# Kernel tuning notes

Hardware: AMD Instinct MI355X
Metric: run time of the kernel (lower is better)

The kernel has to match this reference:

```python
import jax, jax.numpy as jnp
import numpy as np
from math import sqrt

B, S, I, H, O, R = 32, 2048, 128, 512, 64, 1
ALPHA = 0.1


def setup_inputs() -> dict:
    key = jax.random.key(0)
    ks = jax.random.split(key, 7)
    x = jax.random.normal(ks[0], (B, S, I), dtype=jnp.float32)
    input_projective = jax.random.normal(ks[1], (H, R), dtype=jnp.float32) / sqrt(H)
    input_receptive = jax.random.normal(ks[2], (I, R), dtype=jnp.float32) / sqrt(I)
    rec_projective = jax.random.normal(ks[3], (H, R), dtype=jnp.float32) / sqrt(H)
    rec_receptive = jax.random.normal(ks[4], (H, R), dtype=jnp.float32) / sqrt(H)
    bound = 1.0 / sqrt(H)
    readout_w = jax.random.uniform(ks[5], (O, H), minval=-bound, maxval=bound, dtype=jnp.float32)
    readout_b = jax.random.uniform(ks[6], (O,), minval=-bound, maxval=bound, dtype=jnp.float32)
    return {
        "x": x,
        "input_projective": input_projective,
        "input_receptive": input_receptive,
        "rec_projective": rec_projective,
        "rec_receptive": rec_receptive,
        "readout_w": readout_w,
        "readout_b": readout_b,
    }


def reference(x, input_projective, input_receptive, rec_projective, rec_receptive, readout_w, readout_b):
    # Precompute input drive for all steps using the low-rank factorization:
    # x_in[b,s,h] = x[b,s,:] @ input_receptive @ input_projective.T
    x_in = jnp.einsum("bsi,ir,hr->bsh", x, input_receptive, input_projective)

    def step(h, xin_t):
        # r_in = (J @ h.T).T with J = P @ R.T  ->  h @ R @ P.T (low-rank)
        r_in = (h @ rec_receptive) @ rec_projective.T
        dh = -h + jax.nn.relu(r_in + xin_t)  # activation = nlfun (relu)
        h = h + ALPHA * dh                   # Euler hidden update
        out_t = h @ readout_w.T + readout_b
        return h, out_t

    h0 = jnp.zeros((x.shape[0], rec_projective.shape[0]), dtype=x.dtype)
    _, out = jax.lax.scan(step, h0, jnp.swapaxes(x_in, 0, 1))  # scan over time
    return jnp.swapaxes(out, 0, 1)  # [B, S, O]
```

## Files before the change

kernel.cpp:

```cpp
#include <hip/hip_runtime.h>


#define B_ 32
#define S_ 2048
#define I_ 128
#define H_ 512
#define O_ 64

typedef __attribute__((ext_vector_type(8))) short bf16x8;
typedef __attribute__((ext_vector_type(4))) float f32x4;

__device__ __forceinline__ unsigned short f2bf(float f) {
  unsigned int b = __float_as_uint(f);
  b += 0x7FFFu + ((b >> 16) & 1u);
  return (unsigned short)(b >> 16);
}
__device__ __forceinline__ float bf2f(unsigned short s) {
  return __uint_as_float(((unsigned)s) << 16);
}
__device__ __forceinline__ unsigned pack_bf(float lo, float hi) {
  unsigned a = (__float_as_uint(lo) + 0x8000u) >> 16;
  unsigned b = (__float_as_uint(hi) + 0x8000u) & 0xFFFF0000u;
  return a | b;
}

#define DPP_ADD(s, CTRL) \
  s += __int_as_float(__builtin_amdgcn_update_dpp(0, __float_as_int(s), CTRL, 0xF, 0xF, true))

#define RL(s, L) __int_as_float(__builtin_amdgcn_readlane(__float_as_int(s), (L)))

__device__ __forceinline__ void gload16(const void* g, void* l) {
  __builtin_amdgcn_global_load_lds(
      (const __attribute__((address_space(1))) unsigned int*)g,
      (__attribute__((address_space(3))) unsigned int*)l, 16, 0, 0);
}
#define WAITVM(N) asm volatile("s_waitcnt vmcnt(" #N ")" ::: "memory")
#define SCHEDB() __builtin_amdgcn_sched_barrier(0)

#define OFF_SU 0
#define OFF_SV 1920
#define OFF_RP 3456
#define OFF_IP 5504
#define OFF_SW 7552
#define OFF_XS 48512
#define SMEM_BYTES 146816

__device__ __forceinline__ int swz(int row, int col) {
  return row * 64 + (col ^ ((((unsigned)row >> 2) & 3) << 4));
}

__global__ __launch_bounds__(512, 1) void k_fused(
    const float* __restrict__ x, const float* __restrict__ ipj,
    const float* __restrict__ irc, const float* __restrict__ rpj,
    const float* __restrict__ rrc, const float* __restrict__ Wr,
    const float* __restrict__ bias, float* __restrict__ out) {
  extern __shared__ __align__(16) char smem[];
  float* su = (float*)(smem + OFF_SU);
  float* sV = (float*)(smem + OFF_SV);
  float* srp = (float*)(smem + OFF_RP);
  float* sip = (float*)(smem + OFF_IP);
  unsigned short* sw = (unsigned short*)(smem + OFF_SW);
  unsigned short* sBF = (unsigned short*)(smem + OFF_XS);
  float* xsf = (float*)(smem + OFF_XS);

  const int tid = threadIdx.x;
  const int wv = tid >> 6;
  const int lane = tid & 63;
  const int b = blockIdx.x >> 3;
  const int g = blockIdx.x & 7;
  const int r0 = g * 256;

  f32x4 cv0 = *(const f32x4*)(irc + 4 * (lane & 7));
  f32x4 cv1 = *(const f32x4*)(irc + 4 * (lane & 7) + 32);
  f32x4 cv2 = *(const f32x4*)(irc + 4 * (lane & 7) + 64);
  f32x4 cv3 = *(const f32x4*)(irc + 4 * (lane & 7) + 96);
  float rpv[8], ipv[8], rrv[8];
  #pragma unroll
  for (int k = 0; k < 8; k++) {
    int h = lane + 64 * k;
    rpv[k] = rpj[h]; ipv[k] = ipj[h]; rrv[k] = 0.1f * rrc[h];
  }
  if (tid < 96) su[384 + tid] = 0.f;
  if (tid < 80) sV[304 + tid] = 0.f;

#define ISSUE(c) do { \
    int tc_ = r0 - 128 + (c) * 64 + wv * 8; if (tc_ < 0) tc_ = 0; \
    const float* gs_ = x + ((size_t)b * S_ + tc_) * I_ + lane * 4; \
    char* ld_ = (char*)xsf + ((c) % 3) * 32768 + wv * 4096; \
    gload16(gs_,       ld_); \
    gload16(gs_ + 256, ld_ + 1024); \
    gload16(gs_ + 512, ld_ + 2048); \
    gload16(gs_ + 768, ld_ + 3072); \
  } while (0)

#define COMPUTE(c) do { \
    const float* bp_ = xsf + ((c) % 3) * 8192 + (wv * 8 + (lane >> 3)) * 128 + (lane & 7) * 4; \
    f32x4 x0_ = *(const f32x4*)(bp_); \
    f32x4 x1_ = *(const f32x4*)(bp_ + 32); \
    f32x4 x2_ = *(const f32x4*)(bp_ + 64); \
    f32x4 x3_ = *(const f32x4*)(bp_ + 96); \
    float p0_ = x0_[0] * cv0[0], p1_ = x0_[1] * cv0[1]; \
    float p2_ = x0_[2] * cv0[2], p3_ = x0_[3] * cv0[3]; \
    p0_ = fmaf(x1_[0], cv1[0], p0_); p1_ = fmaf(x1_[1], cv1[1], p1_); \
    p2_ = fmaf(x1_[2], cv1[2], p2_); p3_ = fmaf(x1_[3], cv1[3], p3_); \
    p0_ = fmaf(x2_[0], cv2[0], p0_); p1_ = fmaf(x2_[1], cv2[1], p1_); \
    p2_ = fmaf(x2_[2], cv2[2], p2_); p3_ = fmaf(x2_[3], cv2[3], p3_); \
    p0_ = fmaf(x3_[0], cv3[0], p0_); p1_ = fmaf(x3_[1], cv3[1], p1_); \
    p2_ = fmaf(x3_[2], cv3[2], p2_); p3_ = fmaf(x3_[3], cv3[3], p3_); \
    float s_ = (p0_ + p1_) + (p2_ + p3_); \
    DPP_ADD(s_, 0x121); DPP_ADD(s_, 0x122); DPP_ADD(s_, 0x124); \
    float mask_ = (r0 - 128 + (c) * 64 >= 0) ? 1.f : 0.f; \
    if ((lane & 7) == 7) su[(c) * 64 + wv * 8 + (lane >> 3)] = s_ * mask_; \
  } while (0)

  ISSUE(0); ISSUE(1); ISSUE(2);
  WAITVM(8); COMPUTE(0); SCHEDB(); ISSUE(3);
  WAITVM(8); COMPUTE(1); SCHEDB(); ISSUE(4);
  WAITVM(8); COMPUTE(2); SCHEDB(); ISSUE(5);
  WAITVM(8); COMPUTE(3);
  WAITVM(4); COMPUTE(4);
  WAITVM(0); COMPUTE(5);
  __syncthreads();

  float suA = su[32 + wv * 38 + lane];
  float suB = su[32 + wv * 38 + 64 + lane];

  float4 wA0, wB0, wA1, wB1, wA2, wB2, wA3, wB3;
  float4 wA4, wB4, wA5, wB5, wA6, wB6, wA7, wB7;
#define WLOAD(m, A, Bv) do { \
    int seg_ = tid + 512 * (m); \
    int l2_ = seg_ & 63, ot_ = (seg_ >> 6) & 3, kt_ = seg_ >> 8; \
    const float4* wp_ = (const float4*)(Wr + (size_t)(ot_ * 16 + (l2_ & 15)) * H_ + kt_ * 32 + (l2_ >> 4) * 8); \
    A = wp_[0]; Bv = wp_[1]; \
  } while (0)
  WLOAD(0, wA0, wB0); WLOAD(1, wA1, wB1); WLOAD(2, wA2, wB2); WLOAD(3, wA3, wB3);
  WLOAD(4, wA4, wB4); WLOAD(5, wA5, wB5); WLOAD(6, wA6, wB6); WLOAD(7, wA7, wB7);
  float rpa = rpj[tid];
  float ipa = ipj[tid];

#define VSTEP(UT) do { \
    float ut_ = (UT); \
    float q0 = fmaxf(fmaf(v, rpv[0], ut_ * ipv[0]), 0.f) * rrv[0]; \
    float q1 = fmaxf(fmaf(v, rpv[1], ut_ * ipv[1]), 0.f) * rrv[1]; \
    float q2 = fmaxf(fmaf(v, rpv[2], ut_ * ipv[2]), 0.f) * rrv[2]; \
    float q3 = fmaxf(fmaf(v, rpv[3], ut_ * ipv[3]), 0.f) * rrv[3]; \
    float q4 = fmaxf(fmaf(v, rpv[4], ut_ * ipv[4]), 0.f) * rrv[4]; \
    float q5 = fmaxf(fmaf(v, rpv[5], ut_ * ipv[5]), 0.f) * rrv[5]; \
    float q6 = fmaxf(fmaf(v, rpv[6], ut_ * ipv[6]), 0.f) * rrv[6]; \
    float q7 = fmaxf(fmaf(v, rpv[7], ut_ * ipv[7]), 0.f) * rrv[7]; \
    float s_ = ((q0 + q1) + (q2 + q3)) + ((q4 + q5) + (q6 + q7)); \
    DPP_ADD(s_, 0x121); DPP_ADD(s_, 0x122); DPP_ADD(s_, 0x124); DPP_ADD(s_, 0x128); \
    DPP_ADD(s_, 0x142); DPP_ADD(s_, 0x143); \
    float tot_ = RL(s_, 63); \
    v = fmaf(0.9f, v, tot_); \
  } while (0)
  {
    float v = 0.f;
    int base = wv * 38;
    #pragma unroll 8
    for (int i = 0; i < 48; i++) VSTEP(RL(suA, i));
    #pragma unroll 8
    for (int k = 0; k < 16; k++) {
      if (lane == 0) sV[base + k] = v;
      VSTEP(RL(suA, 48 + k));
    }
    #pragma unroll 2
    for (int k = 16; k < 38; k++) {
      if (lane == 0) sV[base + k] = v;
      VSTEP(RL(suB, k - 16));
    }
  }

#define WPACK(m, A, Bv) do { \
    int seg_ = tid + 512 * (m); \
    uint4 pk_; \
    pk_.x = (unsigned)f2bf(A.x) | ((unsigned)f2bf(A.y) << 16); \
    pk_.y = (unsigned)f2bf(A.z) | ((unsigned)f2bf(A.w) << 16); \
    pk_.z = (unsigned)f2bf(Bv.x) | ((unsigned)f2bf(Bv.y) << 16); \
    pk_.w = (unsigned)f2bf(Bv.z) | ((unsigned)f2bf(Bv.w) << 16); \
    *(uint4*)(sBF + seg_ * 8) = pk_; \
  } while (0)
  WPACK(0, wA0, wB0); WPACK(1, wA1, wB1); WPACK(2, wA2, wB2); WPACK(3, wA3, wB3);
  WPACK(4, wA4, wB4); WPACK(5, wA5, wB5); WPACK(6, wA6, wB6); WPACK(7, wA7, wB7);
  srp[tid] = rpa;
  sip[tid] = ipa;
  __syncthreads();

  {
    int tl = lane & 15, quad = lane >> 4;
    float Vr0 = sV[(wv * 3 + 0) * 16 + tl], ur0 = su[80 + (wv * 3 + 0) * 16 + tl];
    float Vr1 = sV[(wv * 3 + 1) * 16 + tl], ur1 = su[80 + (wv * 3 + 1) * 16 + tl];
    float Vr2 = sV[(wv * 3 + 2) * 16 + tl], ur2 = su[80 + (wv * 3 + 2) * 16 + tl];
    f32x4 acc[3][4] = {};
    #pragma unroll 4
    for (int kt = 0; kt < 16; kt++) {
      int hbase = kt * 32 + quad * 8;
      f32x4 rp4a = *(const f32x4*)(srp + hbase);
      f32x4 rp4b = *(const f32x4*)(srp + hbase + 4);
      f32x4 ip4a = *(const f32x4*)(sip + hbase);
      f32x4 ip4b = *(const f32x4*)(sip + hbase + 4);
      bf16x8 bfr0 = *(const bf16x8*)(sBF + (((kt * 4 + 0) * 64 + lane) << 3));
      bf16x8 bfr1 = *(const bf16x8*)(sBF + (((kt * 4 + 1) * 64 + lane) << 3));
      bf16x8 bfr2 = *(const bf16x8*)(sBF + (((kt * 4 + 2) * 64 + lane) << 3));
      bf16x8 bfr3 = *(const bf16x8*)(sBF + (((kt * 4 + 3) * 64 + lane) << 3));
      #pragma unroll
      for (int m = 0; m < 3; m++) {
        float Vm = m == 0 ? Vr0 : (m == 1 ? Vr1 : Vr2);
        float um = m == 0 ? ur0 : (m == 1 ? ur1 : ur2);
        float q[8];
        #pragma unroll
        for (int j = 0; j < 4; j++) {
          q[j]     = fmaxf(fmaf(Vm, rp4a[j], um * ip4a[j]), 0.f);
          q[4 + j] = fmaxf(fmaf(Vm, rp4b[j], um * ip4b[j]), 0.f);
        }
        union { bf16x8 v; unsigned w[4]; } a;
        #pragma unroll
        for (int j = 0; j < 4; j++) a.w[j] = pack_bf(q[2 * j], q[2 * j + 1]);
        acc[m][0] = __builtin_amdgcn_mfma_f32_16x16x32_bf16(a.v, bfr0, acc[m][0], 0, 0, 0);
        acc[m][1] = __builtin_amdgcn_mfma_f32_16x16x32_bf16(a.v, bfr1, acc[m][1], 0, 0, 0);
        acc[m][2] = __builtin_amdgcn_mfma_f32_16x16x32_bf16(a.v, bfr2, acc[m][2], 0, 0, 0);
        acc[m][3] = __builtin_amdgcn_mfma_f32_16x16x32_bf16(a.v, bfr3, acc[m][3], 0, 0, 0);
      }
    }
    #pragma unroll
    for (int m = 0; m < 3; m++) {
      int mt = wv * 3 + m;
      if (mt < 19) {
        int rbase = mt * 16 + quad * 4;
        #pragma unroll
        for (int r = 0; r < 4; r++) {
          #pragma unroll
          for (int ot = 0; ot < 4; ot++)
            sw[swz(rbase + r, ot * 16 + tl)] = f2bf(acc[m][ot][r]);
        }
      }
    }
  }
  __syncthreads();

  {
    float y = 0.f;
    float bo = bias[lane];
    int k0 = wv * 32;
    float* ob = out + ((size_t)(b * S_ + r0 + k0)) * O_ + lane;
    #pragma unroll 8
    for (int i = 0; i < 48; i++)
      y = fmaf(0.9f, y, 0.1f * bf2f(sw[swz(k0 + i, lane)]));
    #pragma unroll 4
    for (int i = 0; i < 32; i++) {
      y = fmaf(0.9f, y, 0.1f * bf2f(sw[swz(k0 + 48 + i, lane)]));
      ob[(size_t)i * O_] = y + bo;
    }
  }
}

extern "C" void kernel_launch(void* const* d_in, const int* in_sizes, int n_in,
                              void* d_out, int out_size, void* d_ws, size_t ws_size,
                              hipStream_t stream) {
  const float* x   = (const float*)d_in[0];
  const float* ipj = (const float*)d_in[1];
  const float* irc = (const float*)d_in[2];
  const float* rpj = (const float*)d_in[3];
  const float* rrc = (const float*)d_in[4];
  const float* Wr  = (const float*)d_in[5];
  const float* br  = (const float*)d_in[6];
  float* out = (float*)d_out;

  static bool s_init = false;
  if (!s_init) {
    hipFuncSetAttribute((const void*)k_fused,
                        hipFuncAttributeMaxDynamicSharedMemorySize, SMEM_BYTES);
    s_init = true;
  }
  k_fused<<<dim3(256), dim3(512), SMEM_BYTES, stream>>>(x, ipj, irc, rpj, rrc,
                                                        Wr, br, out);
}
```

Measured before the change: 116.1 us.

## Split waves: half run longer recurrence chunks, half load and pack weights

```diff
diff --git a/kernel.cpp b/kernel.cpp
--- a/kernel.cpp
+++ b/kernel.cpp
@@ -122,22 +122,9 @@
   WAITVM(0); COMPUTE(5);
   __syncthreads();
 
-  float suA = su[32 + wv * 38 + lane];
-  float suB = su[32 + wv * 38 + 64 + lane];
-
-  float4 wA0, wB0, wA1, wB1, wA2, wB2, wA3, wB3;
-  float4 wA4, wB4, wA5, wB5, wA6, wB6, wA7, wB7;
-#define WLOAD(m, A, Bv) do { \
-    int seg_ = tid + 512 * (m); \
-    int l2_ = seg_ & 63, ot_ = (seg_ >> 6) & 3, kt_ = seg_ >> 8; \
-    const float4* wp_ = (const float4*)(Wr + (size_t)(ot_ * 16 + (l2_ & 15)) * H_ + kt_ * 32 + (l2_ >> 4) * 8); \
-    A = wp_[0]; Bv = wp_[1]; \
-  } while (0)
-  WLOAD(0, wA0, wB0); WLOAD(1, wA1, wB1); WLOAD(2, wA2, wB2); WLOAD(3, wA3, wB3);
-  WLOAD(4, wA4, wB4); WLOAD(5, wA5, wB5); WLOAD(6, wA6, wB6); WLOAD(7, wA7, wB7);
-  float rpa = rpj[tid];
-  float ipa = ipj[tid];
-
+  if (wv < 4) {
+    float suA = su[76 * wv + 32 + lane];
+    float suB = su[76 * wv + 96 + lane];
 #define VSTEP(UT) do { \
     float ut_ = (UT); \
     float q0 = fmaxf(fmaf(v, rpv[0], ut_ * ipv[0]), 0.f) * rrv[0]; \
@@ -154,9 +141,8 @@
     float tot_ = RL(s_, 63); \
     v = fmaf(0.9f, v, tot_); \
   } while (0)
-  {
     float v = 0.f;
-    int base = wv * 38;
+    int base = wv * 76;
     #pragma unroll 8
     for (int i = 0; i < 48; i++) VSTEP(RL(suA, i));
     #pragma unroll 8
@@ -164,26 +150,32 @@
       if (lane == 0) sV[base + k] = v;
       VSTEP(RL(suA, 48 + k));
     }
-    #pragma unroll 2
-    for (int k = 16; k < 38; k++) {
+    #pragma unroll 4
+    for (int k = 16; k < 76; k++) {
       if (lane == 0) sV[base + k] = v;
       VSTEP(RL(suB, k - 16));
     }
-  }
-
-#define WPACK(m, A, Bv) do { \
-    int seg_ = tid + 512 * (m); \
+  } else {
+    int tid2 = tid - 256;
+#define WSEG(m) do { \
+    int seg_ = tid2 + 256 * (m); \
+    int l2_ = seg_ & 63, ot_ = (seg_ >> 6) & 3, kt_ = seg_ >> 8; \
+    const float4* wp_ = (const float4*)(Wr + (size_t)(ot_ * 16 + (l2_ & 15)) * H_ + kt_ * 32 + (l2_ >> 4) * 8); \
+    float4 Wa_ = wp_[0], Wb_ = wp_[1]; \
     uint4 pk_; \
-    pk_.x = (unsigned)f2bf(A.x) | ((unsigned)f2bf(A.y) << 16); \
-    pk_.y = (unsigned)f2bf(A.z) | ((unsigned)f2bf(A.w) << 16); \
-    pk_.z = (unsigned)f2bf(Bv.x) | ((unsigned)f2bf(Bv.y) << 16); \
-    pk_.w = (unsigned)f2bf(Bv.z) | ((unsigned)f2bf(Bv.w) << 16); \
+    pk_.x = (unsigned)f2bf(Wa_.x) | ((unsigned)f2bf(Wa_.y) << 16); \
+    pk_.y = (unsigned)f2bf(Wa_.z) | ((unsigned)f2bf(Wa_.w) << 16); \
+    pk_.z = (unsigned)f2bf(Wb_.x) | ((unsigned)f2bf(Wb_.y) << 16); \
+    pk_.w = (unsigned)f2bf(Wb_.z) | ((unsigned)f2bf(Wb_.w) << 16); \
     *(uint4*)(sBF + seg_ * 8) = pk_; \
   } while (0)
-  WPACK(0, wA0, wB0); WPACK(1, wA1, wB1); WPACK(2, wA2, wB2); WPACK(3, wA3, wB3);
-  WPACK(4, wA4, wB4); WPACK(5, wA5, wB5); WPACK(6, wA6, wB6); WPACK(7, wA7, wB7);
-  srp[tid] = rpa;
-  sip[tid] = ipa;
+    WSEG(0);  WSEG(1);  WSEG(2);  WSEG(3);
+    WSEG(4);  WSEG(5);  WSEG(6);  WSEG(7);
+    WSEG(8);  WSEG(9);  WSEG(10); WSEG(11);
+    WSEG(12); WSEG(13); WSEG(14); WSEG(15);
+    srp[tid2] = rpj[tid2]; srp[tid2 + 256] = rpj[tid2 + 256];
+    sip[tid2] = ipj[tid2]; sip[tid2 + 256] = ipj[tid2 + 256];
+  }
   __syncthreads();
 
   {
```

Measured after the change: 114.3 us. About the same (-1.6%).
